# Optimization experiments

Hardware: AMD Instinct MI355X
Metric: run time of the kernel (lower is better)

The kernel has to match this reference:

```python
import jax, jax.numpy as jnp
import numpy as np
import math

B, S, D, H = 4, 2048, 1024, 16
DEPTH = D // H


def setup_inputs() -> dict:
    key = jax.random.key(0)
    ks = jax.random.split(key, 8)
    scale = 1.0 / math.sqrt(D)
    return {
        "v": jax.random.normal(ks[0], (B, S, D), dtype=jnp.float32),
        "k": jax.random.normal(ks[1], (B, S, D), dtype=jnp.float32),
        "q": jax.random.normal(ks[2], (B, S, D), dtype=jnp.float32),
        "wq_w": jax.random.normal(ks[3], (D, D), dtype=jnp.float32) * scale,
        "wq_b": jnp.zeros((D,), dtype=jnp.float32),
        "wk_w": jax.random.normal(ks[4], (D, D), dtype=jnp.float32) * scale,
        "wk_b": jnp.zeros((D,), dtype=jnp.float32),
        "wv_w": jax.random.normal(ks[5], (D, D), dtype=jnp.float32) * scale,
        "wv_b": jnp.zeros((D,), dtype=jnp.float32),
        "dense_w": jax.random.normal(ks[6], (D, D), dtype=jnp.float32) * scale,
        "dense_b": jnp.zeros((D,), dtype=jnp.float32),
    }


def _split_heads(x):
    # [B, S, D] -> [B, H, S, depth]
    b, s, _ = x.shape
    return x.reshape(b, s, H, DEPTH).transpose(0, 2, 1, 3)


def reference(v, k, q, wq_w, wq_b, wk_w, wk_b, wv_w, wv_b, dense_w, dense_b):
    # Linear projections (torch Linear: x @ W.T + b)
    qh = _split_heads(q @ wq_w.T + wq_b)
    kh = _split_heads(k @ wk_w.T + wk_b)
    vh = _split_heads(v @ wv_w.T + wv_b)

    # scaled dot-product attention; scores: [B, H, S, S]
    scores = jnp.einsum("bhqd,bhkd->bhqk", qh, kh) / math.sqrt(DEPTH)
    attn = jax.nn.softmax(scores, axis=-1)
    ctx = jnp.einsum("bhqk,bhkd->bhqd", attn, vh)

    # merge heads: [B, H, S, depth] -> [B, S, D]
    ctx = ctx.transpose(0, 2, 1, 3).reshape(q.shape[0], -1, D)
    return ctx @ dense_w.T + dense_b
```

## Files before the change

kernel.cpp:

```cpp
#include <hip/hip_runtime.h>
#include <hip/hip_bf16.h>
#include <stdint.h>

#define B_  4
#define S_  2048
#define D_  1024
#define H_  16
#define DP_ 64
#define M_  (B_*S_)

typedef __bf16 bf16x8 __attribute__((ext_vector_type(8)));
typedef float  f32x4  __attribute__((ext_vector_type(4)));
typedef unsigned short u16x8 __attribute__((ext_vector_type(8)));

__device__ __forceinline__ unsigned short f2bf(float f) {
    unsigned u = __builtin_bit_cast(unsigned, f);
    u += 0x7fffu + ((u >> 16) & 1u);
    return (unsigned short)(u >> 16);
}
__device__ __forceinline__ unsigned pk_bf16(float lo, float hi) {
    unsigned a = __builtin_bit_cast(unsigned, lo);
    unsigned b = __builtin_bit_cast(unsigned, hi);
    a += 0x7fffu + ((a >> 16) & 1u);
    b += 0x7fffu + ((b >> 16) & 1u);
    return __builtin_amdgcn_perm(b, a, 0x07060302u);
}
__device__ __forceinline__ bf16x8 ld_frag(const unsigned short* p) {
    return __builtin_bit_cast(bf16x8, *(const u16x8*)p);
}
__device__ __forceinline__ f32x4 mfma16(bf16x8 a, bf16x8 b, f32x4 c) {
    return __builtin_amdgcn_mfma_f32_16x16x32_bf16(a, b, c, 0, 0, 0);
}
__device__ __forceinline__ void gl2lds16(const void* g, void* l) {
    __builtin_amdgcn_global_load_lds(
        (const __attribute__((address_space(1))) unsigned*)g,
        (__attribute__((address_space(3))) unsigned*)l, 16, 0, 0);
}

__global__ __launch_bounds__(256)
void cvt_all(const float* __restrict__ w0, const float* __restrict__ w1,
             const float* __restrict__ w2, const float* __restrict__ w3,
             const float* __restrict__ a0, const float* __restrict__ a1,
             const float* __restrict__ a2,
             unsigned short* __restrict__ Wcat, unsigned short* __restrict__ Acat)
{
    const int gid = blockIdx.x * 256 + threadIdx.x;
    const float* src; unsigned short* dst;
    if (gid < 524288) {
        const int wi = gid >> 17;
        const size_t off = (size_t)(gid & 131071) * 8;
        const float* ws[4] = {w0, w1, w2, w3};
        src = ws[wi] + off; dst = Wcat + (size_t)wi * 1048576 + off;
    } else {
        const int g2 = gid - 524288;
        const int ai = g2 >> 20;
        const size_t off = (size_t)(g2 & 1048575) * 8;
        const float* as[3] = {a0, a1, a2};
        src = as[ai] + off; dst = Acat + (size_t)ai * 8388608 + off;
    }
    float4 x = ((const float4*)src)[0];
    float4 y = ((const float4*)src)[1];
    uint4 o;
    o.x = pk_bf16(x.x, x.y); o.y = pk_bf16(x.z, x.w);
    o.z = pk_bf16(y.x, y.y); o.w = pk_bf16(y.z, y.w);
    *(uint4*)dst = o;
}

template<int MODE>
__global__ __launch_bounds__(256, 3)
void gemm_bt(const unsigned short* __restrict__ Acat, size_t a_stride,
             const unsigned short* __restrict__ Wcat,
             const float* __restrict__ bias0, const float* __restrict__ bias1,
             void* __restrict__ Out)
{
    __shared__ __align__(16) unsigned short SM[16384];
    unsigned short* As = SM;
    unsigned short* Bs = SM + 8192;

    const int z = (MODE == 1) ? blockIdx.z : 0;
    const unsigned short* A = Acat + (size_t)z * a_stride;
    const unsigned short* W = Wcat + ((size_t)z << 20);
    const float* bias = (z == 0) ? bias0 : bias1;

    const int tid  = threadIdx.x;
    const int wave = tid >> 6, lane = tid & 63;
    const int quad = lane >> 4, l16 = lane & 15;
    const int wm = (wave >> 1) * 64, wn = (wave & 1) * 64;
    const int row0 = blockIdx.x * 128, col0 = blockIdx.y * 128;

    const int srow = lane >> 3;
    const int sg   = (lane & 7) ^ srow;

    f32x4 acc[4][4];
#pragma unroll
    for (int i = 0; i < 4; i++)
#pragma unroll
        for (int j = 0; j < 4; j++) acc[i][j] = (f32x4){0.f, 0.f, 0.f, 0.f};

    auto stage = [&](int kt) {
        const int k0 = kt * 64;
#pragma unroll
        for (int j = 0; j < 4; ++j) {
            const int c = wave * 4 + j;
            gl2lds16(A + (size_t)(row0 + c * 8 + srow) * D_ + k0 + sg * 8,
                     (unsigned char*)As + c * 1024);
            gl2lds16(W + (size_t)(col0 + c * 8 + srow) * D_ + k0 + sg * 8,
                     (unsigned char*)Bs + c * 1024);
        }
    };

    stage(0);
    for (int kt = 0; kt < D_ / 64; ++kt) {
        __syncthreads();
        bf16x8 af[4][2], bv[4][2];
#pragma unroll
        for (int mi = 0; mi < 4; ++mi) {
            const int row = wm + mi * 16 + l16;
#pragma unroll
            for (int kd = 0; kd < 2; ++kd)
                af[mi][kd] = ld_frag(&As[row * 64 + (((kd * 4 + quad) ^ (row & 7)) * 8)]);
        }
#pragma unroll
        for (int ni = 0; ni < 4; ++ni) {
            const int row = wn + ni * 16 + l16;
#pragma unroll
            for (int kd = 0; kd < 2; ++kd)
                bv[ni][kd] = ld_frag(&Bs[row * 64 + (((kd * 4 + quad) ^ (row & 7)) * 8)]);
        }
        if (kt + 1 < D_ / 64) {
            __syncthreads();
            stage(kt + 1);
        }
#pragma unroll
        for (int kd = 0; kd < 2; ++kd)
#pragma unroll
            for (int mi = 0; mi < 4; ++mi)
#pragma unroll
                for (int ni = 0; ni < 4; ++ni) {
                    if (MODE == 1)
                        acc[mi][ni] = mfma16(bv[ni][kd], af[mi][kd], acc[mi][ni]);
                    else
                        acc[mi][ni] = mfma16(af[mi][kd], bv[ni][kd], acc[mi][ni]);
                }
    }

    if constexpr (MODE == 1) {
        unsigned short* Lt = SM;
        unsigned short* OutQK = (unsigned short*)Out + ((size_t)z << 23);
        const int bidx = row0 >> 11;
        const float scale = (z == 0) ? 0.18033688f : 1.0f;
#pragma unroll
        for (int hc = 0; hc < 2; ++hc) {
            __syncthreads();
            if ((wave & 1) == hc) {
#pragma unroll
                for (int ni = 0; ni < 4; ++ni) {
                    const int c_loc = wn + ni * 16 + quad * 4;
                    const float4 bb = *(const float4*)&bias[col0 + c_loc];
#pragma unroll
                    for (int mi = 0; mi < 4; ++mi) {
                        const int s_loc = wm + mi * 16 + l16;
                        uint2 w;
                        w.x = pk_bf16((acc[mi][ni][0] + bb.x) * scale,
                                      (acc[mi][ni][1] + bb.y) * scale);
                        w.y = pk_bf16((acc[mi][ni][2] + bb.z) * scale,
                                      (acc[mi][ni][3] + bb.w) * scale);
                        *(uint2*)&Lt[s_loc * 72 + (c_loc & 63)] = w;
                    }
                }
            }
            __syncthreads();
            const int hg = (col0 >> 6) + hc;
            const size_t qb = (size_t)(bidx * H_ + hg) * S_ + (row0 & (S_ - 1));
#pragma unroll
            for (int p = 0; p < 4; ++p) {
                const int s = p * 32 + (tid >> 3);
                const int g = tid & 7;
                uint4 d = *(const uint4*)&Lt[s * 72 + g * 8];
                *(uint4*)(OutQK + (qb + s) * DP_ + g * 8) = d;
            }
        }
        return;
    }
    if constexpr (MODE == 2) {
        unsigned short* Lt = SM;
        unsigned short* OutV = (unsigned short*)Out;
        const int bidx = row0 >> 11;
#pragma unroll
        for (int hc = 0; hc < 2; ++hc) {
            __syncthreads();
            if ((wave & 1) == hc) {
#pragma unroll
                for (int ni = 0; ni < 4; ++ni) {
                    const float bvv = bias0[col0 + hc * 64 + ni * 16 + l16];
#pragma unroll
                    for (int mi = 0; mi < 4; ++mi) {
                        uint2 w;
                        w.x = pk_bf16(acc[mi][ni][0] + bvv, acc[mi][ni][1] + bvv);
                        w.y = pk_bf16(acc[mi][ni][2] + bvv, acc[mi][ni][3] + bvv);
                        *(uint2*)&Lt[(ni * 16 + l16) * 132 + wm + mi * 16 + quad * 4] = w;
                    }
                }
            }
            __syncthreads();
            const int hg = (col0 >> 6) + hc;
            const size_t vb = ((size_t)(bidx * H_ + hg) * DP_) * S_;
#pragma unroll
            for (int p = 0; p < 4; ++p) {
                const int dpl = p * 16 + (tid >> 4);
                uint4 d = *(const uint4*)&Lt[dpl * 132 + (tid & 15) * 8];
                *(uint4*)(OutV + vb + (size_t)dpl * S_ + (row0 & (S_ - 1)) + (tid & 15) * 8) = d;
            }
        }
        return;
    }
#pragma unroll
    for (int ni = 0; ni < 4; ni++) {
        const int col = col0 + wn + ni * 16 + l16;
        const float bvv = bias0[col];
#pragma unroll
        for (int mi = 0; mi < 4; mi++) {
            const int rowb = row0 + wm + mi * 16 + quad * 4;
#pragma unroll
            for (int r = 0; r < 4; r++)
                ((float*)Out)[(size_t)(rowb + r) * D_ + col] = acc[mi][ni][r] + bvv;
        }
    }
}

__global__ __launch_bounds__(256)
void flash_attn(const unsigned short* __restrict__ Qh,
                const unsigned short* __restrict__ Kh,
                const unsigned short* __restrict__ Vtg,
                unsigned short* __restrict__ Ctx)
{
    constexpr int LP = 40;
    __shared__ __align__(16) unsigned short Kt[128 * 64];
    __shared__ __align__(16) unsigned short Vt[64 * 128];

    const int tid  = threadIdx.x;
    const int wave = tid >> 6, lane = tid & 63;
    const int quad = lane >> 4, l16 = lane & 15;
    const int bh = blockIdx.x, qt = blockIdx.y;
    const size_t base = (size_t)bh * S_ * DP_;

    bf16x8 qf[2][2];
#pragma unroll
    for (int mi = 0; mi < 2; mi++)
#pragma unroll
        for (int kd = 0; kd < 2; kd++)
            qf[mi][kd] = ld_frag(&Qh[base + (size_t)(qt * 128 + wave * 32 + mi * 16 + l16) * DP_ + kd * 32 + quad * 8]);

    f32x4 o[2][4];
    float lsum[2] = {0.f, 0.f};
#pragma unroll
    for (int mi = 0; mi < 2; mi++)
#pragma unroll
        for (int nd = 0; nd < 4; nd++) o[mi][nd] = (f32x4){0.f, 0.f, 0.f, 0.f};

    unsigned short* pw = Kt + wave * 32 * LP;
    const int kswz = ((lane & 7) ^ (lane >> 3)) * 8;
    const int vdp_l = lane >> 4;
    const int vslot = lane & 15;

    for (int t = 0; t < S_ / 128; ++t) {
        __syncthreads();
#pragma unroll
        for (int j = 0; j < 4; ++j) {
            const int ck = wave * 4 + j;
            gl2lds16(Kh + base + (size_t)(t * 128 + ck * 8 + (lane >> 3)) * DP_ + kswz,
                     (unsigned char*)Kt + ck * 1024);
            const int dp = ck * 4 + vdp_l;
            gl2lds16(Vtg + base + (size_t)dp * S_ + t * 128 + ((vslot ^ (dp & 15)) * 8),
                     (unsigned char*)Vt + ck * 1024);
        }
        __syncthreads();

        f32x4 st[8][2];
#pragma unroll
        for (int kb = 0; kb < 8; ++kb) { st[kb][0] = (f32x4){0,0,0,0}; st[kb][1] = (f32x4){0,0,0,0}; }
#pragma unroll
        for (int kb = 0; kb < 8; ++kb) {
            const int krow = (kb * 16 + l16) * 64;
            bf16x8 kf0 = ld_frag(&Kt[krow + (((quad)     ^ (l16 & 7)) * 8)]);
            bf16x8 kf1 = ld_frag(&Kt[krow + (((4 + quad) ^ (l16 & 7)) * 8)]);
            st[kb][0] = mfma16(kf0, qf[0][0], st[kb][0]);
            st[kb][0] = mfma16(kf1, qf[0][1], st[kb][0]);
            st[kb][1] = mfma16(kf0, qf[1][0], st[kb][1]);
            st[kb][1] = mfma16(kf1, qf[1][1], st[kb][1]);
        }

        __syncthreads();

#pragma unroll
        for (int ch = 0; ch < 4; ++ch) {
#pragma unroll
            for (int kk = 0; kk < 2; ++kk)
#pragma unroll
                for (int mi = 0; mi < 2; ++mi) {
                    f32x4 s = st[2 * ch + kk][mi];
                    float p0 = __builtin_amdgcn_exp2f(s[0]);
                    float p1 = __builtin_amdgcn_exp2f(s[1]);
                    float p2 = __builtin_amdgcn_exp2f(s[2]);
                    float p3 = __builtin_amdgcn_exp2f(s[3]);
                    lsum[mi] += (p0 + p1) + (p2 + p3);
                    uint2 w;
                    w.x = pk_bf16(p0, p1);
                    w.y = pk_bf16(p2, p3);
                    *(uint2*)&pw[(mi * 16 + l16) * LP + kk * 16 + quad * 4] = w;
                }
            asm volatile("s_waitcnt lgkmcnt(0)" ::: "memory");
            bf16x8 pa0 = ld_frag(&pw[(l16)      * LP + quad * 8]);
            bf16x8 pa1 = ld_frag(&pw[(16 + l16) * LP + quad * 8]);
#pragma unroll
            for (int nd = 0; nd < 4; ++nd) {
                const int dp = nd * 16 + l16;
                bf16x8 vbf = ld_frag(&Vt[dp * 128 + (((ch * 4 + quad) ^ l16) * 8)]);
                o[0][nd] = mfma16(pa0, vbf, o[0][nd]);
                o[1][nd] = mfma16(pa1, vbf, o[1][nd]);
            }
            asm volatile("" ::: "memory");
        }
    }

#pragma unroll
    for (int mi = 0; mi < 2; ++mi) {
        lsum[mi] += __shfl_xor(lsum[mi], 16, 64);
        lsum[mi] += __shfl_xor(lsum[mi], 32, 64);
    }

    const int b = bh >> 4, h = bh & 15;
#pragma unroll
    for (int mi = 0; mi < 2; ++mi)
#pragma unroll
        for (int r = 0; r < 4; ++r) {
            const float lT  = __shfl(lsum[mi], quad * 4 + r, 64);
            const float inv = __builtin_amdgcn_rcpf(lT);
            const int srw = qt * 128 + wave * 32 + mi * 16 + quad * 4 + r;
#pragma unroll
            for (int nd = 0; nd < 4; ++nd)
                Ctx[((size_t)(b * S_ + srw)) * D_ + h * DP_ + nd * 16 + l16] = f2bf(o[mi][nd][r] * inv);
        }
}

extern "C" void kernel_launch(void* const* d_in, const int* in_sizes, int n_in,
                              void* d_out, int out_size, void* d_ws, size_t ws_size,
                              hipStream_t stream)
{
    const float* v    = (const float*)d_in[0];
    const float* k    = (const float*)d_in[1];
    const float* q    = (const float*)d_in[2];
    const float* wq_w = (const float*)d_in[3];
    const float* wq_b = (const float*)d_in[4];
    const float* wk_w = (const float*)d_in[5];
    const float* wk_b = (const float*)d_in[6];
    const float* wv_w = (const float*)d_in[7];
    const float* wv_b = (const float*)d_in[8];
    const float* dw   = (const float*)d_in[9];
    const float* db   = (const float*)d_in[10];
    float* out = (float*)d_out;

    unsigned short* Qh   = (unsigned short*)d_ws;
    unsigned short* Kh   = Qh   + (size_t)M_ * D_;
    unsigned short* Vt   = Kh   + (size_t)M_ * D_;
    unsigned short* Ctx  = Vt   + (size_t)M_ * D_;
    unsigned short* Wcat = Ctx  + (size_t)M_ * D_;
    unsigned short* Acat = Wcat + (size_t)4 * D_ * D_;

    cvt_all<<<14336, 256, 0, stream>>>(wq_w, wk_w, wv_w, dw, q, k, v, Wcat, Acat);

    dim3 blk(256);
    gemm_bt<1><<<dim3(M_ / 128, D_ / 128, 2), blk, 0, stream>>>(
        Acat, (size_t)M_ * D_, Wcat, wq_b, wk_b, Qh);
    gemm_bt<2><<<dim3(M_ / 128, D_ / 128, 1), blk, 0, stream>>>(
        Acat + (size_t)2 * M_ * D_, 0, Wcat + (size_t)2 * D_ * D_, wv_b, wv_b, Vt);

    flash_attn<<<dim3(B_ * H_, S_ / 128), blk, 0, stream>>>(Qh, Kh, Vt, Ctx);

    gemm_bt<0><<<dim3(M_ / 128, D_ / 128, 1), blk, 0, stream>>>(
        Ctx, 0, Wcat + (size_t)3 * D_ * D_, db, db, out);
}
```

Before: 366.3 us.

## Merge QKV projection launches, use hardware bf16 convert, add MFMA priority hints

The separate Q/K and V projection GEMM launches are merged into one launch with a z dimension of 3, and z selects the epilogue layout (head-split rows or transposed V). Software round-to-nearest bf16 packing is replaced with compiler vector conversion, which can lower to the native packed convert instruction. The attention kernel gains an occupancy hint of 4 blocks, s_setprio around its MFMA sections, and a two-lane partial row-sum accumulator. The merged launch removes one kernel boundary and tail, but it brings a runtime branch on z into a shared kernel and may raise register pressure.

Result: slower. 503.6 us (+37.5%).

```diff
diff --git a/kernel.cpp b/kernel.cpp
--- a/kernel.cpp
+++ b/kernel.cpp
@@ -10,20 +10,19 @@
 #define M_  (B_*S_)
 
 typedef __bf16 bf16x8 __attribute__((ext_vector_type(8)));
+typedef __bf16 bf16x2_t __attribute__((ext_vector_type(2)));
 typedef float  f32x4  __attribute__((ext_vector_type(4)));
+typedef float  f32x2_t __attribute__((ext_vector_type(2)));
 typedef unsigned short u16x8 __attribute__((ext_vector_type(8)));
 
 __device__ __forceinline__ unsigned short f2bf(float f) {
-    unsigned u = __builtin_bit_cast(unsigned, f);
-    u += 0x7fffu + ((u >> 16) & 1u);
-    return (unsigned short)(u >> 16);
+    __bf16 b = (__bf16)f;
+    return __builtin_bit_cast(unsigned short, b);
 }
 __device__ __forceinline__ unsigned pk_bf16(float lo, float hi) {
-    unsigned a = __builtin_bit_cast(unsigned, lo);
-    unsigned b = __builtin_bit_cast(unsigned, hi);
-    a += 0x7fffu + ((a >> 16) & 1u);
-    b += 0x7fffu + ((b >> 16) & 1u);
-    return __builtin_amdgcn_perm(b, a, 0x07060302u);
+    f32x2_t f = {lo, hi};
+    bf16x2_t b = __builtin_convertvector(f, bf16x2_t);
+    return __builtin_bit_cast(unsigned, b);
 }
 __device__ __forceinline__ bf16x8 ld_frag(const unsigned short* p) {
     return __builtin_bit_cast(bf16x8, *(const u16x8*)p);
@@ -71,16 +70,17 @@
 void gemm_bt(const unsigned short* __restrict__ Acat, size_t a_stride,
              const unsigned short* __restrict__ Wcat,
              const float* __restrict__ bias0, const float* __restrict__ bias1,
-             void* __restrict__ Out)
+             const float* __restrict__ bias2,
+             void* __restrict__ Out, void* __restrict__ Out2)
 {
     __shared__ __align__(16) unsigned short SM[16384];
     unsigned short* As = SM;
     unsigned short* Bs = SM + 8192;
 
-    const int z = (MODE == 1) ? blockIdx.z : 0;
+    const int z = (MODE == 3) ? blockIdx.z : 0;
     const unsigned short* A = Acat + (size_t)z * a_stride;
     const unsigned short* W = Wcat + ((size_t)z << 20);
-    const float* bias = (z == 0) ? bias0 : bias1;
+    const float* bias = (z == 0) ? bias0 : (z == 1 ? bias1 : bias2);
 
     const int tid  = threadIdx.x;
     const int wave = tid >> 6, lane = tid & 63;
@@ -109,6 +109,8 @@
         }
     };
 
+    const bool swapped = (MODE == 3) && (z < 2);
+
     stage(0);
     for (int kt = 0; kt < D_ / 64; ++kt) {
         __syncthreads();
@@ -137,79 +139,79 @@
             for (int mi = 0; mi < 4; ++mi)
 #pragma unroll
                 for (int ni = 0; ni < 4; ++ni) {
-                    if (MODE == 1)
+                    if (swapped)
                         acc[mi][ni] = mfma16(bv[ni][kd], af[mi][kd], acc[mi][ni]);
                     else
                         acc[mi][ni] = mfma16(af[mi][kd], bv[ni][kd], acc[mi][ni]);
                 }
     }
 
-    if constexpr (MODE == 1) {
-        unsigned short* Lt = SM;
-        unsigned short* OutQK = (unsigned short*)Out + ((size_t)z << 23);
-        const int bidx = row0 >> 11;
-        const float scale = (z == 0) ? 0.18033688f : 1.0f;
-#pragma unroll
-        for (int hc = 0; hc < 2; ++hc) {
-            __syncthreads();
-            if ((wave & 1) == hc) {
-#pragma unroll
-                for (int ni = 0; ni < 4; ++ni) {
-                    const int c_loc = wn + ni * 16 + quad * 4;
-                    const float4 bb = *(const float4*)&bias[col0 + c_loc];
-#pragma unroll
-                    for (int mi = 0; mi < 4; ++mi) {
-                        const int s_loc = wm + mi * 16 + l16;
-                        uint2 w;
-                        w.x = pk_bf16((acc[mi][ni][0] + bb.x) * scale,
-                                      (acc[mi][ni][1] + bb.y) * scale);
-                        w.y = pk_bf16((acc[mi][ni][2] + bb.z) * scale,
-                                      (acc[mi][ni][3] + bb.w) * scale);
-                        *(uint2*)&Lt[s_loc * 72 + (c_loc & 63)] = w;
+    if constexpr (MODE == 3) {
+        if (z < 2) {
+            unsigned short* Lt = SM;
+            unsigned short* OutQK = (unsigned short*)Out + ((size_t)z << 23);
+            const int bidx = row0 >> 11;
+            const float scale = (z == 0) ? 0.18033688f : 1.0f;
+#pragma unroll
+            for (int hc = 0; hc < 2; ++hc) {
+                __syncthreads();
+                if ((wave & 1) == hc) {
+#pragma unroll
+                    for (int ni = 0; ni < 4; ++ni) {
+                        const int c_loc = wn + ni * 16 + quad * 4;
+                        const float4 bb = *(const float4*)&bias[col0 + c_loc];
+#pragma unroll
+                        for (int mi = 0; mi < 4; ++mi) {
+                            const int s_loc = wm + mi * 16 + l16;
+                            uint2 w;
+                            w.x = pk_bf16((acc[mi][ni][0] + bb.x) * scale,
+                                          (acc[mi][ni][1] + bb.y) * scale);
+                            w.y = pk_bf16((acc[mi][ni][2] + bb.z) * scale,
+                                          (acc[mi][ni][3] + bb.w) * scale);
+                            *(uint2*)&Lt[s_loc * 72 + (c_loc & 63)] = w;
+                        }
                     }
                 }
+                __syncthreads();
+                const int hg = (col0 >> 6) + hc;
+                const size_t qb = (size_t)(bidx * H_ + hg) * S_ + (row0 & (S_ - 1));
+#pragma unroll
+                for (int p = 0; p < 4; ++p) {
+                    const int s = p * 32 + (tid >> 3);
+                    const int g = tid & 7;
+                    uint4 d = *(const uint4*)&Lt[s * 72 + g * 8];
+                    *(uint4*)(OutQK + (qb + s) * DP_ + g * 8) = d;
+                }
             }
-            __syncthreads();
-            const int hg = (col0 >> 6) + hc;
-            const size_t qb = (size_t)(bidx * H_ + hg) * S_ + (row0 & (S_ - 1));
-#pragma unroll
-            for (int p = 0; p < 4; ++p) {
-                const int s = p * 32 + (tid >> 3);
-                const int g = tid & 7;
-                uint4 d = *(const uint4*)&Lt[s * 72 + g * 8];
-                *(uint4*)(OutQK + (qb + s) * DP_ + g * 8) = d;
-            }
-        }
-        return;
-    }
-    if constexpr (MODE == 2) {
-        unsigned short* Lt = SM;
-        unsigned short* OutV = (unsigned short*)Out;
-        const int bidx = row0 >> 11;
-#pragma unroll
-        for (int hc = 0; hc < 2; ++hc) {
-            __syncthreads();
-            if ((wave & 1) == hc) {
-#pragma unroll
-                for (int ni = 0; ni < 4; ++ni) {
-                    const float bvv = bias0[col0 + hc * 64 + ni * 16 + l16];
-#pragma unroll
-                    for (int mi = 0; mi < 4; ++mi) {
-                        uint2 w;
-                        w.x = pk_bf16(acc[mi][ni][0] + bvv, acc[mi][ni][1] + bvv);
-                        w.y = pk_bf16(acc[mi][ni][2] + bvv, acc[mi][ni][3] + bvv);
-                        *(uint2*)&Lt[(ni * 16 + l16) * 132 + wm + mi * 16 + quad * 4] = w;
+        } else {
+            unsigned short* Lt = SM;
+            unsigned short* OutV = (unsigned short*)Out2;
+            const int bidx = row0 >> 11;
+#pragma unroll
+            for (int hc = 0; hc < 2; ++hc) {
+                __syncthreads();
+                if ((wave & 1) == hc) {
+#pragma unroll
+                    for (int ni = 0; ni < 4; ++ni) {
+                        const float bvv = bias[col0 + hc * 64 + ni * 16 + l16];
+#pragma unroll
+                        for (int mi = 0; mi < 4; ++mi) {
+                            uint2 w;
+                            w.x = pk_bf16(acc[mi][ni][0] + bvv, acc[mi][ni][1] + bvv);
+                            w.y = pk_bf16(acc[mi][ni][2] + bvv, acc[mi][ni][3] + bvv);
+                            *(uint2*)&Lt[(ni * 16 + l16) * 132 + wm + mi * 16 + quad * 4] = w;
+                        }
                     }
                 }
-            }
-            __syncthreads();
-            const int hg = (col0 >> 6) + hc;
-            const size_t vb = ((size_t)(bidx * H_ + hg) * DP_) * S_;
-#pragma unroll
-            for (int p = 0; p < 4; ++p) {
-                const int dpl = p * 16 + (tid >> 4);
-                uint4 d = *(const uint4*)&Lt[dpl * 132 + (tid & 15) * 8];
-                *(uint4*)(OutV + vb + (size_t)dpl * S_ + (row0 & (S_ - 1)) + (tid & 15) * 8) = d;
+                __syncthreads();
+                const int hg = (col0 >> 6) + hc;
+                const size_t vb = ((size_t)(bidx * H_ + hg) * DP_) * S_;
+#pragma unroll
+                for (int p = 0; p < 4; ++p) {
+                    const int dpl = p * 16 + (tid >> 4);
+                    uint4 d = *(const uint4*)&Lt[dpl * 132 + (tid & 15) * 8];
+                    *(uint4*)(OutV + vb + (size_t)dpl * S_ + (row0 & (S_ - 1)) + (tid & 15) * 8) = d;
+                }
             }
         }
         return;
@@ -228,7 +230,7 @@
     }
 }
 
-__global__ __launch_bounds__(256)
+__global__ __launch_bounds__(256, 4)
 void flash_attn(const unsigned short* __restrict__ Qh,
                 const unsigned short* __restrict__ Kh,
                 const unsigned short* __restrict__ Vtg,
@@ -252,7 +254,7 @@
             qf[mi][kd] = ld_frag(&Qh[base + (size_t)(qt * 128 + wave * 32 + mi * 16 + l16) * DP_ + kd * 32 + quad * 8]);
 
     f32x4 o[2][4];
-    float lsum[2] = {0.f, 0.f};
+    f32x2_t ls[2] = {(f32x2_t){0.f, 0.f}, (f32x2_t){0.f, 0.f}};
 #pragma unroll
     for (int mi = 0; mi < 2; mi++)
 #pragma unroll
@@ -279,6 +281,7 @@
         f32x4 st[8][2];
 #pragma unroll
         for (int kb = 0; kb < 8; ++kb) { st[kb][0] = (f32x4){0,0,0,0}; st[kb][1] = (f32x4){0,0,0,0}; }
+        __builtin_amdgcn_s_setprio(1);
 #pragma unroll
         for (int kb = 0; kb < 8; ++kb) {
             const int krow = (kb * 16 + l16) * 64;
@@ -289,6 +292,7 @@
             st[kb][1] = mfma16(kf0, qf[1][0], st[kb][1]);
             st[kb][1] = mfma16(kf1, qf[1][1], st[kb][1]);
         }
+        __builtin_amdgcn_s_setprio(0);
 
         __syncthreads();
 
@@ -303,7 +307,8 @@
                     float p1 = __builtin_amdgcn_exp2f(s[1]);
                     float p2 = __builtin_amdgcn_exp2f(s[2]);
                     float p3 = __builtin_amdgcn_exp2f(s[3]);
-                    lsum[mi] += (p0 + p1) + (p2 + p3);
+                    ls[mi] += (f32x2_t){p0, p2};
+                    ls[mi] += (f32x2_t){p1, p3};
                     uint2 w;
                     w.x = pk_bf16(p0, p1);
                     w.y = pk_bf16(p2, p3);
@@ -312,6 +317,7 @@
             asm volatile("s_waitcnt lgkmcnt(0)" ::: "memory");
             bf16x8 pa0 = ld_frag(&pw[(l16)      * LP + quad * 8]);
             bf16x8 pa1 = ld_frag(&pw[(16 + l16) * LP + quad * 8]);
+            __builtin_amdgcn_s_setprio(1);
 #pragma unroll
             for (int nd = 0; nd < 4; ++nd) {
                 const int dp = nd * 16 + l16;
@@ -319,12 +325,15 @@
                 o[0][nd] = mfma16(pa0, vbf, o[0][nd]);
                 o[1][nd] = mfma16(pa1, vbf, o[1][nd]);
             }
+            __builtin_amdgcn_s_setprio(0);
             asm volatile("" ::: "memory");
         }
     }
 
+    float lsum[2];
 #pragma unroll
     for (int mi = 0; mi < 2; ++mi) {
+        lsum[mi] = ls[mi][0] + ls[mi][1];
         lsum[mi] += __shfl_xor(lsum[mi], 16, 64);
         lsum[mi] += __shfl_xor(lsum[mi], 32, 64);
     }
@@ -370,13 +379,11 @@
     cvt_all<<<14336, 256, 0, stream>>>(wq_w, wk_w, wv_w, dw, q, k, v, Wcat, Acat);
 
     dim3 blk(256);
-    gemm_bt<1><<<dim3(M_ / 128, D_ / 128, 2), blk, 0, stream>>>(
-        Acat, (size_t)M_ * D_, Wcat, wq_b, wk_b, Qh);
-    gemm_bt<2><<<dim3(M_ / 128, D_ / 128, 1), blk, 0, stream>>>(
-        Acat + (size_t)2 * M_ * D_, 0, Wcat + (size_t)2 * D_ * D_, wv_b, wv_b, Vt);
+    gemm_bt<3><<<dim3(M_ / 128, D_ / 128, 3), blk, 0, stream>>>(
+        Acat, (size_t)M_ * D_, Wcat, wq_b, wk_b, wv_b, Qh, Vt);
 
     flash_attn<<<dim3(B_ * H_, S_ / 128), blk, 0, stream>>>(Qh, Kh, Vt, Ctx);
 
     gemm_bt<0><<<dim3(M_ / 128, D_ / 128, 1), blk, 0, stream>>>(
-        Ctx, 0, Wcat + (size_t)3 * D_ * D_, db, db, out);
-}
+        Ctx, 0, Wcat + (size_t)3 * D_ * D_, db, db, db, out, nullptr);
+}
```
